# Kernel optimization log

Hardware: AMD Instinct MI355X
Metric: run time of the kernel (lower is better)

The kernel has to match this reference:

```python
import jax, jax.numpy as jnp
import numpy as np

N = 262144
DIM = 256
NUM_HEADS = 4
HEAD_DIM = DIM // NUM_HEADS
B = 4096
SCALE = HEAD_DIM ** (-0.5)
EPS = 1e-8


def setup_inputs() -> dict:
    key = jax.random.key(0)
    ks = jax.random.split(key, 7)
    x = jax.random.normal(ks[0], (N, DIM), dtype=jnp.float32)
    batch = jnp.sort(jax.random.randint(ks[1], (N,), 0, B)).astype(jnp.int64)
    query = jax.random.normal(ks[2], (NUM_HEADS, HEAD_DIM), dtype=jnp.float32)
    # nn.Linear default init scale ~ 1/sqrt(dim); keep exp() well-behaved
    key_w = jax.random.normal(ks[3], (DIM, DIM), dtype=jnp.float32) / np.sqrt(DIM)
    key_b = jax.random.normal(ks[4], (DIM,), dtype=jnp.float32) * 0.01
    value_w = jax.random.normal(ks[5], (DIM, DIM), dtype=jnp.float32) / np.sqrt(DIM)
    value_b = jax.random.normal(ks[6], (DIM,), dtype=jnp.float32) * 0.01
    return {"x": x, "batch": batch, "query": query, "key_w": key_w,
            "key_b": key_b, "value_w": value_w, "value_b": value_b}


def reference(x, batch, query, key_w, key_b, value_w, value_b):
    # k, v: [N, H, Hd]  (torch Linear: x @ W.T + b)
    k = (x @ key_w.T + key_b).reshape(N, NUM_HEADS, HEAD_DIM)
    v = (x @ value_w.T + value_b).reshape(N, NUM_HEADS, HEAD_DIM)
    # attn: [N, H] -- dot of learned per-head query with each node's key
    attn = jnp.einsum('hd,nhd->nh', query, k) * SCALE
    attn_exp = jnp.exp(attn)  # faithful: no max-subtraction in original
    # segment softmax denominator gathered back to nodes: [N, H]
    attn_sum = jax.ops.segment_sum(attn_exp, batch, num_segments=B)[batch]
    attn_norm = attn_exp / (attn_sum + EPS)
    # weighted values scatter-added per segment: [B, H, Hd]
    weighted = attn_norm[:, :, None] * v
    pooled = jax.ops.segment_sum(weighted, batch, num_segments=B)
    return pooled.reshape(B, DIM)
```

## Files before the change

### kernel.cpp

```cpp
#include <hip/hip_runtime.h>


constexpr int DIM = 256;
constexpr int NH  = 4;
constexpr int HD  = 64;
constexpr int G   = 8;
constexpr float SCL  = 0.125f;
constexpr float EPSV = 1e-8f;

constexpr int WS_QW   = 0;
constexpr int WS_QB   = 1024;
constexpr int WS_OFFS = 1088;
constexpr int WS_VWT  = 8192;

template<int CTRL>
__device__ __forceinline__ float dpp_ror_add(float v){
  int r = __builtin_amdgcn_update_dpp(0, __float_as_int(v), CTRL, 0xF, 0xF, false);
  return v + __int_as_float(r);
}
__device__ __forceinline__ float red32(float v){
  v = dpp_ror_add<0x121>(v);
  v = dpp_ror_add<0x122>(v);
  v = dpp_ror_add<0x124>(v);
  v = dpp_ror_add<0x128>(v);
  int r = __builtin_amdgcn_ds_swizzle(__float_as_int(v), 0x401F);
  return v + __int_as_float(r);
}

__global__ void prep_seg(const float* __restrict__ query,
                         const float* __restrict__ key_w,
                         const float* __restrict__ key_b,
                         const float* __restrict__ value_w,
                         const int* __restrict__ batch32,
                         float* __restrict__ ws,
                         int* __restrict__ offs,
                         int N, int B, int do_vwt){
  const int bid = blockIdx.x, tid = threadIdx.x;
  if (bid < 64){
    if (do_vwt){
      float4 v = *(const float4*)(value_w + (size_t)tid*DIM + 4*bid);
      ((float4*)(ws + WS_VWT))[bid*256 + tid] = v;
    }
  } else if (bid < 68){
    int t = (bid - 64)*256 + tid;
    int h = t >> 8, j = t & 255;
    float acc = 0.f;
    #pragma unroll 8
    for (int d = 0; d < HD; ++d)
      acc += query[h*HD+d] * key_w[(size_t)(h*HD+d)*DIM + j];
    ws[WS_QW + t] = acc;
    if (j == 0){
      float bb = 0.f;
      for (int d = 0; d < HD; ++d)
        bb += query[h*HD+d] * key_b[h*HD+d];
      ws[WS_QB + h] = bb;
    }
  } else {
    int i = (bid - 68)*256 + tid;
    if (i >= N) return;
    const bool is64 = (batch32[N-1] == 0);
    int v  = is64 ? batch32[2*i] : batch32[i];
    int vp = (i == 0) ? -1 : (is64 ? batch32[2*(i-1)] : batch32[i-1]);
    for (int b = vp + 1; b <= v; ++b) offs[b] = i;
    if (i == N-1)
      for (int b = v + 1; b <= B; ++b) offs[b] = N;
  }
}

__global__ __launch_bounds__(512, 4)
void attn_g8(const float* __restrict__ x,
             const int* __restrict__ offs,
             const float* __restrict__ ws,
             const float* __restrict__ value_b,
             float* __restrict__ out){
  __shared__ __align__(16) float S_all[8][1024];
  __shared__ __align__(16) float Sfin[G][1024];
  __shared__ float sums_all[8][NH];
  __shared__ float invs[G][NH], wsums[G][NH];

  const int b0  = blockIdx.x * G;
  const int tid = threadIdx.x;
  const int wave = tid >> 6, lane = tid & 63;
  const int half = lane >> 5, sl = lane & 31;
  const int sigma = wave * 2 + half;

  float qwr[NH][8];
  #pragma unroll
  for (int h = 0; h < NH; ++h){
    float4 a = *(const float4*)(ws + WS_QW + h*DIM + 4*sl);
    float4 c = *(const float4*)(ws + WS_QW + h*DIM + 128 + 4*sl);
    qwr[h][0]=a.x; qwr[h][1]=a.y; qwr[h][2]=a.z; qwr[h][3]=a.w;
    qwr[h][4]=c.x; qwr[h][5]=c.y; qwr[h][6]=c.z; qwr[h][7]=c.w;
  }
  float qb[NH];
  #pragma unroll
  for (int h = 0; h < NH; ++h) qb[h] = ws[WS_QB + h];

  const float4* xr4 = (const float4*)x;
  const float4 Z = make_float4(0.f, 0.f, 0.f, 0.f);

  for (int g = 0; g < G; ++g){
    const int s = offs[b0 + g], e = offs[b0 + g + 1];

    float Sacc[NH][8];
    #pragma unroll
    for (int h = 0; h < NH; ++h)
      #pragma unroll
      for (int c = 0; c < 8; ++c) Sacc[h][c] = 0.f;
    float se[NH] = {0.f, 0.f, 0.f, 0.f};

    int n0 = s + sigma*2;
    bool v0 = n0 < e;
    bool v1 = n0 + 1 < e;
    float4 la0=Z, lb0=Z, la1=Z, lb1=Z;
    if (v0){ la0 = xr4[(size_t)n0*64 + sl];     lb0 = xr4[(size_t)n0*64 + 32 + sl]; }
    if (v1){ la1 = xr4[(size_t)(n0+1)*64 + sl]; lb1 = xr4[(size_t)(n0+1)*64 + 32 + sl]; }

    while (v0){
      const int nn = n0 + 32;
      const bool w0 = nn < e;
      const bool w1 = nn + 1 < e;
      float4 nc0=Z, nd0=Z, nc1=Z, nd1=Z;
      if (w0){ nc0 = xr4[(size_t)nn*64 + sl];     nd0 = xr4[(size_t)nn*64 + 32 + sl]; }
      if (w1){ nc1 = xr4[(size_t)(nn+1)*64 + sl]; nd1 = xr4[(size_t)(nn+1)*64 + 32 + sl]; }

      float xv0[8] = {la0.x,la0.y,la0.z,la0.w,lb0.x,lb0.y,lb0.z,lb0.w};
      float xv1[8] = {la1.x,la1.y,la1.z,la1.w,lb1.x,lb1.y,lb1.z,lb1.w};

      float p0[NH], p1[NH];
      #pragma unroll
      for (int h = 0; h < NH; ++h){
        float s0 = 0.f, s1 = 0.f;
        #pragma unroll
        for (int c = 0; c < 8; ++c){ s0 += qwr[h][c]*xv0[c]; s1 += qwr[h][c]*xv1[c]; }
        p0[h] = s0; p1[h] = s1;
      }
      #pragma unroll
      for (int h = 0; h < NH; ++h){
        p0[h] = red32(p0[h]);
        p1[h] = red32(p1[h]);
      }
      const float g1 = v1 ? 1.f : 0.f;
      #pragma unroll
      for (int h = 0; h < NH; ++h){
        float e0 = __expf((p0[h] + qb[h]) * SCL);
        float e1 = __expf((p1[h] + qb[h]) * SCL) * g1;
        se[h] += e0 + e1;
        #pragma unroll
        for (int c = 0; c < 8; ++c)
          Sacc[h][c] += e0*xv0[c] + e1*xv1[c];
      }
      n0 = nn; v0 = w0; v1 = w1;
      la0 = nc0; lb0 = nd0; la1 = nc1; lb1 = nd1;
    }

    #pragma unroll
    for (int h = 0; h < NH; ++h){
      se[h] += __shfl_xor(se[h], 32, 64);
      #pragma unroll
      for (int c = 0; c < 8; ++c) Sacc[h][c] += __shfl_xor(Sacc[h][c], 32, 64);
    }
    if (half == 0){
      #pragma unroll
      for (int h = 0; h < NH; ++h){
        float4 lo = make_float4(Sacc[h][0], Sacc[h][1], Sacc[h][2], Sacc[h][3]);
        float4 hi = make_float4(Sacc[h][4], Sacc[h][5], Sacc[h][6], Sacc[h][7]);
        *(float4*)&S_all[wave][h*DIM + 4*sl]       = lo;
        *(float4*)&S_all[wave][h*DIM + 128 + 4*sl] = hi;
      }
      if (sl == 0){
        #pragma unroll
        for (int h = 0; h < NH; ++h) sums_all[wave][h] = se[h];
      }
    }
    __syncthreads();

    #pragma unroll
    for (int k2 = 0; k2 < 2; ++k2){
      const int idx = tid + k2*512;
      float sv = 0.f;
      #pragma unroll
      for (int w = 0; w < 8; ++w) sv += S_all[w][idx];
      Sfin[g][idx] = sv;
    }
    if (tid < NH){
      float tot = 0.f;
      #pragma unroll
      for (int w = 0; w < 8; ++w) tot += sums_all[w][tid];
      float inv = 1.f / (tot + EPSV);
      invs[g][tid]  = inv;
      wsums[g][tid] = tot * inv;
    }
    __syncthreads();
  }

  const int t = tid & 255, part = tid >> 8, h = t >> 6;
  const float4* vwt4 = (const float4*)(ws + WS_VWT);
  float acc[G];
  #pragma unroll
  for (int g = 0; g < G; ++g) acc[g] = 0.f;

  #pragma unroll 4
  for (int jj = part*32; jj < part*32 + 32; ++jj){
    const float4 w4 = vwt4[jj*256 + t];
    #pragma unroll
    for (int g = 0; g < G; ++g){
      const float4 s4 = *(const float4*)&Sfin[g][h*256 + 4*jj];
      acc[g] += w4.x*s4.x + w4.y*s4.y + w4.z*s4.z + w4.w*s4.w;
    }
  }
  float* ep = &S_all[0][0];
  #pragma unroll
  for (int g = 0; g < G; ++g) ep[(part*G + g)*256 + t] = acc[g];
  __syncthreads();
  if (part == 0){
    const float vb = value_b[t];
    #pragma unroll
    for (int g = 0; g < G; ++g){
      out[(size_t)(b0 + g)*256 + t] =
          (ep[g*256 + t] + ep[(G + g)*256 + t]) * invs[g][h] + wsums[g][h] * vb;
    }
  }
}

__global__ __launch_bounds__(512, 4)
void attn_pool_fused(const float* __restrict__ x,
                     const int* __restrict__ offs,
                     const float* __restrict__ ws,
                     const float* __restrict__ value_w,
                     const float* __restrict__ value_b,
                     float* __restrict__ out){
  __shared__ __align__(16) float lds[8192 + 32 + 1024 + 512 + 8];
  float* S_all    = lds;
  float* sums_all = lds + 8192;

  const int b   = blockIdx.x;
  const int tid = threadIdx.x;
  const int seg_start = offs[b];
  const int seg_end   = offs[b+1];

  const int wave = tid >> 6, lane = tid & 63;
  const int half = lane >> 5, sl = lane & 31;
  const int sigma = wave * 2 + half;

  float qwr[NH][8];
  #pragma unroll
  for (int h = 0; h < NH; ++h){
    float4 a = *(const float4*)(ws + WS_QW + h*DIM + 4*sl);
    float4 c = *(const float4*)(ws + WS_QW + h*DIM + 128 + 4*sl);
    qwr[h][0]=a.x; qwr[h][1]=a.y; qwr[h][2]=a.z; qwr[h][3]=a.w;
    qwr[h][4]=c.x; qwr[h][5]=c.y; qwr[h][6]=c.z; qwr[h][7]=c.w;
  }
  float qb[NH];
  #pragma unroll
  for (int h = 0; h < NH; ++h) qb[h] = ws[WS_QB + h];

  float Sacc[NH][8];
  #pragma unroll
  for (int h = 0; h < NH; ++h)
    #pragma unroll
    for (int c = 0; c < 8; ++c) Sacc[h][c] = 0.f;
  float se[NH] = {0.f, 0.f, 0.f, 0.f};

  const float4* xr4 = (const float4*)x;
  const float4 Z = make_float4(0.f,0.f,0.f,0.f);

  int n0 = seg_start + sigma*2;
  bool v0 = n0 < seg_end;
  bool v1 = n0 + 1 < seg_end;
  float4 a0=Z, b0=Z, a1=Z, b1=Z;
  if (v0){ a0 = xr4[(size_t)n0*64 + sl];     b0 = xr4[(size_t)n0*64 + 32 + sl]; }
  if (v1){ a1 = xr4[(size_t)(n0+1)*64 + sl]; b1 = xr4[(size_t)(n0+1)*64 + 32 + sl]; }

  while (v0){
    const int nn = n0 + 32;
    const bool w0 = nn < seg_end;
    const bool w1 = nn + 1 < seg_end;
    float4 c0=Z, d0=Z, c1=Z, d1=Z;
    if (w0){ c0 = xr4[(size_t)nn*64 + sl];     d0 = xr4[(size_t)nn*64 + 32 + sl]; }
    if (w1){ c1 = xr4[(size_t)(nn+1)*64 + sl]; d1 = xr4[(size_t)(nn+1)*64 + 32 + sl]; }

    float xv0[8] = {a0.x,a0.y,a0.z,a0.w,b0.x,b0.y,b0.z,b0.w};
    float xv1[8] = {a1.x,a1.y,a1.z,a1.w,b1.x,b1.y,b1.z,b1.w};

    float p0[NH], p1[NH];
    #pragma unroll
    for (int h = 0; h < NH; ++h){
      float s0 = 0.f, s1 = 0.f;
      #pragma unroll
      for (int c = 0; c < 8; ++c){ s0 += qwr[h][c]*xv0[c]; s1 += qwr[h][c]*xv1[c]; }
      p0[h] = s0; p1[h] = s1;
    }
    #pragma unroll
    for (int m = 1; m < 32; m <<= 1){
      #pragma unroll
      for (int h = 0; h < NH; ++h){
        p0[h] += __shfl_xor(p0[h], m, 64);
        p1[h] += __shfl_xor(p1[h], m, 64);
      }
    }
    const float g1 = v1 ? 1.f : 0.f;
    #pragma unroll
    for (int h = 0; h < NH; ++h){
      float e0 = __expf((p0[h] + qb[h]) * SCL);
      float e1 = __expf((p1[h] + qb[h]) * SCL) * g1;
      se[h] += e0 + e1;
      #pragma unroll
      for (int c = 0; c < 8; ++c)
        Sacc[h][c] += e0*xv0[c] + e1*xv1[c];
    }
    n0 = nn; v0 = w0; v1 = w1;
    a0 = c0; b0 = d0; a1 = c1; b1 = d1;
  }

  #pragma unroll
  for (int h = 0; h < NH; ++h){
    se[h] += __shfl_xor(se[h], 32, 64);
    #pragma unroll
    for (int c = 0; c < 8; ++c) Sacc[h][c] += __shfl_xor(Sacc[h][c], 32, 64);
  }
  if (half == 0){
    #pragma unroll
    for (int h = 0; h < NH; ++h){
      float4 lo = make_float4(Sacc[h][0], Sacc[h][1], Sacc[h][2], Sacc[h][3]);
      float4 hi = make_float4(Sacc[h][4], Sacc[h][5], Sacc[h][6], Sacc[h][7]);
      *(float4*)&S_all[wave*1024 + h*DIM + 4*sl]       = lo;
      *(float4*)&S_all[wave*1024 + h*DIM + 128 + 4*sl] = hi;
    }
    if (sl == 0){
      #pragma unroll
      for (int h = 0; h < NH; ++h) sums_all[wave*4 + h] = se[h];
    }
  }
  __syncthreads();

  float* Sfin  = lds + 8224;
  float* invs  = lds + 9760;
  float* wsums = invs + 4;
  #pragma unroll
  for (int k = 0; k < 2; ++k){
    const int idx = tid + k*512;
    float sv = 0.f;
    #pragma unroll
    for (int w = 0; w < 8; ++w) sv += S_all[w*1024 + idx];
    Sfin[idx] = sv;
  }
  if (tid < NH){
    float tot = 0.f;
    #pragma unroll
    for (int w = 0; w < 8; ++w) tot += sums_all[w*4 + tid];
    float inv = 1.f / (tot + EPSV);
    invs[tid] = inv; wsums[tid] = tot * inv;
  }
  __syncthreads();

  float* ep2 = lds + 9248;
  const int t = tid & 255, part = tid >> 8;
  const int h2 = t >> 6;
  const float4* vrow = (const float4*)(value_w + (size_t)t * DIM) + part*32;
  const float4* sp   = (const float4*)&Sfin[h2*256] + part*32;
  float acc = 0.f;
  #pragma unroll
  for (int q = 0; q < 32; ++q){
    float4 r = vrow[q];
    float4 sv = sp[q];
    acc += r.x*sv.x + r.y*sv.y + r.z*sv.z + r.w*sv.w;
  }
  ep2[part*256 + t] = acc;
  __syncthreads();
  if (part == 0)
    out[(size_t)b * DIM + t] = (ep2[t] + ep2[256 + t]) * invs[h2] + wsums[h2] * value_b[t];
}

extern "C" void kernel_launch(void* const* d_in, const int* in_sizes, int n_in,
                              void* d_out, int out_size, void* d_ws, size_t ws_size,
                              hipStream_t stream){
  const float* x       = (const float*)d_in[0];
  const int*   batch   = (const int*)d_in[1];
  const float* query   = (const float*)d_in[2];
  const float* key_w   = (const float*)d_in[3];
  const float* key_b   = (const float*)d_in[4];
  const float* value_w = (const float*)d_in[5];
  const float* value_b = (const float*)d_in[6];
  float* ws  = (float*)d_ws;
  float* out = (float*)d_out;

  const int N = in_sizes[1];
  const int B = out_size / DIM;

  int* offs = (int*)(ws + WS_OFFS);

  const size_t need_vwt = ((size_t)WS_VWT + 65536) * sizeof(float);
  const int do_vwt = (ws_size >= need_vwt) ? 1 : 0;

  const int seg_blocks = (N + 255) / 256;
  prep_seg<<<68 + seg_blocks, 256, 0, stream>>>(query, key_w, key_b, value_w,
                                                batch, ws, offs, N, B, do_vwt);
  if (do_vwt && (B % G) == 0)
    attn_g8<<<B / G, 512, 0, stream>>>(x, offs, ws, value_b, out);
  else
    attn_pool_fused<<<B, 512, 0, stream>>>(x, offs, ws, value_w, value_b, out);
}
```

Measured before the change: 402.2 us.

## Fuse prep into single attention kernel with per-block binary search and qW recompute

Replaces the prep kernel plus grouped attention kernel with a single kernel that finds segment offsets by binary search over the batch array, recomputes query·key_w into LDS per block, and reads value_w rows directly instead of a transposed workspace copy. This removes one kernel launch and the global offset and transpose passes. In exchange every block redundantly computes the 1024-element qW product (64 MACs per element, reading key_w), and value_w is now read row-wise per thread, which is uncoalesced. The fallback path also switches to the DPP reduction.

```diff
diff --git a/kernel.cpp b/kernel.cpp
--- a/kernel.cpp
+++ b/kernel.cpp
@@ -4,14 +4,12 @@
 constexpr int DIM = 256;
 constexpr int NH  = 4;
 constexpr int HD  = 64;
-constexpr int G   = 8;
 constexpr float SCL  = 0.125f;
 constexpr float EPSV = 1e-8f;
 
 constexpr int WS_QW   = 0;
 constexpr int WS_QB   = 1024;
 constexpr int WS_OFFS = 1088;
-constexpr int WS_VWT  = 8192;
 
 template<int CTRL>
 __device__ __forceinline__ float dpp_ror_add(float v){
@@ -27,22 +25,209 @@
   return v + __int_as_float(r);
 }
 
+__global__ __launch_bounds__(512, 4)
+void attn_all(const float* __restrict__ x,
+              const int* __restrict__ batch32,
+              const float* __restrict__ query,
+              const float* __restrict__ key_w,
+              const float* __restrict__ key_b,
+              const float* __restrict__ value_w,
+              const float* __restrict__ value_b,
+              float* __restrict__ out,
+              int N, int B){
+  constexpr int G8 = 8;
+  __shared__ __align__(16) float S_all[8][1024];
+  __shared__ __align__(16) float Sfin[G8][1024];
+  __shared__ __align__(16) float qwL[1024];
+  __shared__ float qbL[NH];
+  __shared__ float sums_all[8][NH];
+  __shared__ float invs[G8][NH], wsums[G8][NH];
+  __shared__ int offsL[G8 + 1];
+
+  const int bid = blockIdx.x, tid = threadIdx.x;
+  const int b0  = bid * G8;
+
+  const bool is64 = (batch32[N-1] == 0);
+  if (tid <= G8){
+    const int target = b0 + tid;
+    int lo = 0, hi = N;
+    while (lo < hi){
+      const int mid = (lo + hi) >> 1;
+      const int v = is64 ? batch32[2*(size_t)mid] : batch32[mid];
+      if (v < target) lo = mid + 1; else hi = mid;
+    }
+    offsL[tid] = lo;
+  }
+
+  for (int idx = tid; idx < 1024; idx += 512){
+    const int h = idx >> 8, j = idx & 255;
+    float acc = 0.f;
+    #pragma unroll 8
+    for (int d = 0; d < HD; ++d)
+      acc += query[h*HD+d] * key_w[(size_t)(h*HD+d)*DIM + j];
+    qwL[idx] = acc;
+  }
+  if (tid < NH){
+    float bb = 0.f;
+    for (int d = 0; d < HD; ++d)
+      bb += query[tid*HD+d] * key_b[tid*HD+d];
+    qbL[tid] = bb;
+  }
+  __syncthreads();
+
+  const int wave = tid >> 6, lane = tid & 63;
+  const int half = lane >> 5, sl = lane & 31;
+  const int sigma = wave * 2 + half;
+
+  float qwr[NH][8];
+  #pragma unroll
+  for (int h = 0; h < NH; ++h){
+    float4 a = *(const float4*)&qwL[h*DIM + 4*sl];
+    float4 c = *(const float4*)&qwL[h*DIM + 128 + 4*sl];
+    qwr[h][0]=a.x; qwr[h][1]=a.y; qwr[h][2]=a.z; qwr[h][3]=a.w;
+    qwr[h][4]=c.x; qwr[h][5]=c.y; qwr[h][6]=c.z; qwr[h][7]=c.w;
+  }
+  float qb[NH];
+  #pragma unroll
+  for (int h = 0; h < NH; ++h) qb[h] = qbL[h];
+
+  const float4* xr4 = (const float4*)x;
+  const float4 Z = make_float4(0.f, 0.f, 0.f, 0.f);
+
+  for (int g = 0; g < G8; ++g){
+    const int s = offsL[g], e = offsL[g+1];
+
+    float Sacc[NH][8];
+    #pragma unroll
+    for (int h = 0; h < NH; ++h)
+      #pragma unroll
+      for (int c = 0; c < 8; ++c) Sacc[h][c] = 0.f;
+    float se[NH] = {0.f, 0.f, 0.f, 0.f};
+
+    int n0 = s + sigma*2;
+    bool v0 = n0 < e;
+    bool v1 = n0 + 1 < e;
+    float4 la0=Z, lb0=Z, la1=Z, lb1=Z;
+    if (v0){ la0 = xr4[(size_t)n0*64 + sl];     lb0 = xr4[(size_t)n0*64 + 32 + sl]; }
+    if (v1){ la1 = xr4[(size_t)(n0+1)*64 + sl]; lb1 = xr4[(size_t)(n0+1)*64 + 32 + sl]; }
+
+    while (v0){
+      const int nn = n0 + 32;
+      const bool w0 = nn < e;
+      const bool w1 = nn + 1 < e;
+      float4 nc0=Z, nd0=Z, nc1=Z, nd1=Z;
+      if (w0){ nc0 = xr4[(size_t)nn*64 + sl];     nd0 = xr4[(size_t)nn*64 + 32 + sl]; }
+      if (w1){ nc1 = xr4[(size_t)(nn+1)*64 + sl]; nd1 = xr4[(size_t)(nn+1)*64 + 32 + sl]; }
+
+      float xv0[8] = {la0.x,la0.y,la0.z,la0.w,lb0.x,lb0.y,lb0.z,lb0.w};
+      float xv1[8] = {la1.x,la1.y,la1.z,la1.w,lb1.x,lb1.y,lb1.z,lb1.w};
+
+      float p0[NH], p1[NH];
+      #pragma unroll
+      for (int h = 0; h < NH; ++h){
+        float s0 = 0.f, s1 = 0.f;
+        #pragma unroll
+        for (int c = 0; c < 8; ++c){ s0 += qwr[h][c]*xv0[c]; s1 += qwr[h][c]*xv1[c]; }
+        p0[h] = s0; p1[h] = s1;
+      }
+      #pragma unroll
+      for (int h = 0; h < NH; ++h){
+        p0[h] = red32(p0[h]);
+        p1[h] = red32(p1[h]);
+      }
+      const float g1 = v1 ? 1.f : 0.f;
+      #pragma unroll
+      for (int h = 0; h < NH; ++h){
+        float e0 = __expf((p0[h] + qb[h]) * SCL);
+        float e1 = __expf((p1[h] + qb[h]) * SCL) * g1;
+        se[h] += e0 + e1;
+        #pragma unroll
+        for (int c = 0; c < 8; ++c)
+          Sacc[h][c] += e0*xv0[c] + e1*xv1[c];
+      }
+      n0 = nn; v0 = w0; v1 = w1;
+      la0 = nc0; lb0 = nd0; la1 = nc1; lb1 = nd1;
+    }
+
+    #pragma unroll
+    for (int h = 0; h < NH; ++h){
+      se[h] += __shfl_xor(se[h], 32, 64);
+      #pragma unroll
+      for (int c = 0; c < 8; ++c) Sacc[h][c] += __shfl_xor(Sacc[h][c], 32, 64);
+    }
+    if (half == 0){
+      #pragma unroll
+      for (int h = 0; h < NH; ++h){
+        float4 lo = make_float4(Sacc[h][0], Sacc[h][1], Sacc[h][2], Sacc[h][3]);
+        float4 hi = make_float4(Sacc[h][4], Sacc[h][5], Sacc[h][6], Sacc[h][7]);
+        *(float4*)&S_all[wave][h*DIM + 4*sl]       = lo;
+        *(float4*)&S_all[wave][h*DIM + 128 + 4*sl] = hi;
+      }
+      if (sl == 0){
+        #pragma unroll
+        for (int h = 0; h < NH; ++h) sums_all[wave][h] = se[h];
+      }
+    }
+    __syncthreads();
+
+    #pragma unroll
+    for (int k2 = 0; k2 < 2; ++k2){
+      const int idx = tid + k2*512;
+      float sv = 0.f;
+      #pragma unroll
+      for (int w = 0; w < 8; ++w) sv += S_all[w][idx];
+      Sfin[g][idx] = sv;
+    }
+    if (tid < NH){
+      float tot = 0.f;
+      #pragma unroll
+      for (int w = 0; w < 8; ++w) tot += sums_all[w][tid];
+      float inv = 1.f / (tot + EPSV);
+      invs[g][tid]  = inv;
+      wsums[g][tid] = tot * inv;
+    }
+    __syncthreads();
+  }
+
+  const int t = tid & 255, part = tid >> 8, h = t >> 6;
+  const float4* vrow = (const float4*)(value_w + (size_t)t * DIM) + part*32;
+  float acc[G8];
+  #pragma unroll
+  for (int g = 0; g < G8; ++g) acc[g] = 0.f;
+
+  for (int q = 0; q < 32; ++q){
+    const float4 r = vrow[q];
+    const int jj = part*32 + q;
+    #pragma unroll
+    for (int g = 0; g < G8; ++g){
+      const float4 s4 = *(const float4*)&Sfin[g][h*256 + 4*jj];
+      acc[g] += r.x*s4.x + r.y*s4.y + r.z*s4.z + r.w*s4.w;
+    }
+  }
+  float* ep = &S_all[0][0];
+  #pragma unroll
+  for (int g = 0; g < G8; ++g) ep[(part*G8 + g)*256 + t] = acc[g];
+  __syncthreads();
+  if (part == 0){
+    const float vb = value_b[t];
+    #pragma unroll
+    for (int g = 0; g < G8; ++g){
+      out[(size_t)(b0 + g)*256 + t] =
+          (ep[g*256 + t] + ep[(G8 + g)*256 + t]) * invs[g][h] + wsums[g][h] * vb;
+    }
+  }
+}
+
 __global__ void prep_seg(const float* __restrict__ query,
                          const float* __restrict__ key_w,
                          const float* __restrict__ key_b,
-                         const float* __restrict__ value_w,
                          const int* __restrict__ batch32,
                          float* __restrict__ ws,
                          int* __restrict__ offs,
-                         int N, int B, int do_vwt){
+                         int N, int B){
   const int bid = blockIdx.x, tid = threadIdx.x;
-  if (bid < 64){
-    if (do_vwt){
-      float4 v = *(const float4*)(value_w + (size_t)tid*DIM + 4*bid);
-      ((float4*)(ws + WS_VWT))[bid*256 + tid] = v;
-    }
-  } else if (bid < 68){
-    int t = (bid - 64)*256 + tid;
+  if (bid < 4){
+    int t = bid*256 + tid;
     int h = t >> 8, j = t & 255;
     float acc = 0.f;
     #pragma unroll 8
@@ -56,7 +241,7 @@
       ws[WS_QB + h] = bb;
     }
   } else {
-    int i = (bid - 68)*256 + tid;
+    int i = (bid - 4)*256 + tid;
     if (i >= N) return;
     const bool is64 = (batch32[N-1] == 0);
     int v  = is64 ? batch32[2*i] : batch32[i];
@@ -64,162 +249,6 @@
     for (int b = vp + 1; b <= v; ++b) offs[b] = i;
     if (i == N-1)
       for (int b = v + 1; b <= B; ++b) offs[b] = N;
-  }
-}
-
-__global__ __launch_bounds__(512, 4)
-void attn_g8(const float* __restrict__ x,
-             const int* __restrict__ offs,
-             const float* __restrict__ ws,
-             const float* __restrict__ value_b,
-             float* __restrict__ out){
-  __shared__ __align__(16) float S_all[8][1024];
-  __shared__ __align__(16) float Sfin[G][1024];
-  __shared__ float sums_all[8][NH];
-  __shared__ float invs[G][NH], wsums[G][NH];
-
-  const int b0  = blockIdx.x * G;
-  const int tid = threadIdx.x;
-  const int wave = tid >> 6, lane = tid & 63;
-  const int half = lane >> 5, sl = lane & 31;
-  const int sigma = wave * 2 + half;
-
-  float qwr[NH][8];
-  #pragma unroll
-  for (int h = 0; h < NH; ++h){
-    float4 a = *(const float4*)(ws + WS_QW + h*DIM + 4*sl);
-    float4 c = *(const float4*)(ws + WS_QW + h*DIM + 128 + 4*sl);
-    qwr[h][0]=a.x; qwr[h][1]=a.y; qwr[h][2]=a.z; qwr[h][3]=a.w;
-    qwr[h][4]=c.x; qwr[h][5]=c.y; qwr[h][6]=c.z; qwr[h][7]=c.w;
-  }
-  float qb[NH];
-  #pragma unroll
-  for (int h = 0; h < NH; ++h) qb[h] = ws[WS_QB + h];
-
-  const float4* xr4 = (const float4*)x;
-  const float4 Z = make_float4(0.f, 0.f, 0.f, 0.f);
-
-  for (int g = 0; g < G; ++g){
-    const int s = offs[b0 + g], e = offs[b0 + g + 1];
-
-    float Sacc[NH][8];
-    #pragma unroll
-    for (int h = 0; h < NH; ++h)
-      #pragma unroll
-      for (int c = 0; c < 8; ++c) Sacc[h][c] = 0.f;
-    float se[NH] = {0.f, 0.f, 0.f, 0.f};
-
-    int n0 = s + sigma*2;
-    bool v0 = n0 < e;
-    bool v1 = n0 + 1 < e;
-    float4 la0=Z, lb0=Z, la1=Z, lb1=Z;
-    if (v0){ la0 = xr4[(size_t)n0*64 + sl];     lb0 = xr4[(size_t)n0*64 + 32 + sl]; }
-    if (v1){ la1 = xr4[(size_t)(n0+1)*64 + sl]; lb1 = xr4[(size_t)(n0+1)*64 + 32 + sl]; }
-
-    while (v0){
-      const int nn = n0 + 32;
-      const bool w0 = nn < e;
-      const bool w1 = nn + 1 < e;
-      float4 nc0=Z, nd0=Z, nc1=Z, nd1=Z;
-      if (w0){ nc0 = xr4[(size_t)nn*64 + sl];     nd0 = xr4[(size_t)nn*64 + 32 + sl]; }
-      if (w1){ nc1 = xr4[(size_t)(nn+1)*64 + sl]; nd1 = xr4[(size_t)(nn+1)*64 + 32 + sl]; }
-
-      float xv0[8] = {la0.x,la0.y,la0.z,la0.w,lb0.x,lb0.y,lb0.z,lb0.w};
-      float xv1[8] = {la1.x,la1.y,la1.z,la1.w,lb1.x,lb1.y,lb1.z,lb1.w};
-
-      float p0[NH], p1[NH];
-      #pragma unroll
-      for (int h = 0; h < NH; ++h){
-        float s0 = 0.f, s1 = 0.f;
-        #pragma unroll
-        for (int c = 0; c < 8; ++c){ s0 += qwr[h][c]*xv0[c]; s1 += qwr[h][c]*xv1[c]; }
-        p0[h] = s0; p1[h] = s1;
-      }
-      #pragma unroll
-      for (int h = 0; h < NH; ++h){
-        p0[h] = red32(p0[h]);
-        p1[h] = red32(p1[h]);
-      }
-      const float g1 = v1 ? 1.f : 0.f;
-      #pragma unroll
-      for (int h = 0; h < NH; ++h){
-        float e0 = __expf((p0[h] + qb[h]) * SCL);
-        float e1 = __expf((p1[h] + qb[h]) * SCL) * g1;
-        se[h] += e0 + e1;
-        #pragma unroll
-        for (int c = 0; c < 8; ++c)
-          Sacc[h][c] += e0*xv0[c] + e1*xv1[c];
-      }
-      n0 = nn; v0 = w0; v1 = w1;
-      la0 = nc0; lb0 = nd0; la1 = nc1; lb1 = nd1;
-    }
-
-    #pragma unroll
-    for (int h = 0; h < NH; ++h){
-      se[h] += __shfl_xor(se[h], 32, 64);
-      #pragma unroll
-      for (int c = 0; c < 8; ++c) Sacc[h][c] += __shfl_xor(Sacc[h][c], 32, 64);
-    }
-    if (half == 0){
-      #pragma unroll
-      for (int h = 0; h < NH; ++h){
-        float4 lo = make_float4(Sacc[h][0], Sacc[h][1], Sacc[h][2], Sacc[h][3]);
-        float4 hi = make_float4(Sacc[h][4], Sacc[h][5], Sacc[h][6], Sacc[h][7]);
-        *(float4*)&S_all[wave][h*DIM + 4*sl]       = lo;
-        *(float4*)&S_all[wave][h*DIM + 128 + 4*sl] = hi;
-      }
-      if (sl == 0){
-        #pragma unroll
-        for (int h = 0; h < NH; ++h) sums_all[wave][h] = se[h];
-      }
-    }
-    __syncthreads();
-
-    #pragma unroll
-    for (int k2 = 0; k2 < 2; ++k2){
-      const int idx = tid + k2*512;
-      float sv = 0.f;
-      #pragma unroll
-      for (int w = 0; w < 8; ++w) sv += S_all[w][idx];
-      Sfin[g][idx] = sv;
-    }
-    if (tid < NH){
-      float tot = 0.f;
-      #pragma unroll
-      for (int w = 0; w < 8; ++w) tot += sums_all[w][tid];
-      float inv = 1.f / (tot + EPSV);
-      invs[g][tid]  = inv;
-      wsums[g][tid] = tot * inv;
-    }
-    __syncthreads();
-  }
-
-  const int t = tid & 255, part = tid >> 8, h = t >> 6;
-  const float4* vwt4 = (const float4*)(ws + WS_VWT);
-  float acc[G];
-  #pragma unroll
-  for (int g = 0; g < G; ++g) acc[g] = 0.f;
-
-  #pragma unroll 4
-  for (int jj = part*32; jj < part*32 + 32; ++jj){
-    const float4 w4 = vwt4[jj*256 + t];
-    #pragma unroll
-    for (int g = 0; g < G; ++g){
-      const float4 s4 = *(const float4*)&Sfin[g][h*256 + 4*jj];
-      acc[g] += w4.x*s4.x + w4.y*s4.y + w4.z*s4.z + w4.w*s4.w;
-    }
-  }
-  float* ep = &S_all[0][0];
-  #pragma unroll
-  for (int g = 0; g < G; ++g) ep[(part*G + g)*256 + t] = acc[g];
-  __syncthreads();
-  if (part == 0){
-    const float vb = value_b[t];
-    #pragma unroll
-    for (int g = 0; g < G; ++g){
-      out[(size_t)(b0 + g)*256 + t] =
-          (ep[g*256 + t] + ep[(G + g)*256 + t]) * invs[g][h] + wsums[g][h] * vb;
-    }
   }
 }
 
@@ -292,12 +321,9 @@
       p0[h] = s0; p1[h] = s1;
     }
     #pragma unroll
-    for (int m = 1; m < 32; m <<= 1){
-      #pragma unroll
-      for (int h = 0; h < NH; ++h){
-        p0[h] += __shfl_xor(p0[h], m, 64);
-        p1[h] += __shfl_xor(p1[h], m, 64);
-      }
+    for (int h = 0; h < NH; ++h){
+      p0[h] = red32(p0[h]);
+      p1[h] = red32(p1[h]);
     }
     const float g1 = v1 ? 1.f : 0.f;
     #pragma unroll
@@ -385,19 +411,17 @@
   float* ws  = (float*)d_ws;
   float* out = (float*)d_out;
 
-  const int N = in_sizes[1];
-  const int B = out_size / DIM;
-
-  int* offs = (int*)(ws + WS_OFFS);
-
-  const size_t need_vwt = ((size_t)WS_VWT + 65536) * sizeof(float);
-  const int do_vwt = (ws_size >= need_vwt) ? 1 : 0;
-
-  const int seg_blocks = (N + 255) / 256;
-  prep_seg<<<68 + seg_blocks, 256, 0, stream>>>(query, key_w, key_b, value_w,
-                                                batch, ws, offs, N, B, do_vwt);
-  if (do_vwt && (B % G) == 0)
-    attn_g8<<<B / G, 512, 0, stream>>>(x, offs, ws, value_b, out);
-  else
+  int N = in_sizes[1];
+  int B = out_size / DIM;
+
+  if ((B % 8) == 0){
+    attn_all<<<B / 8, 512, 0, stream>>>(x, batch, query, key_w, key_b,
+                                        value_w, value_b, out, N, B);
+  } else {
+    int* offs = (int*)(ws + WS_OFFS);
+    const int seg_blocks = (N + 255) / 256;
+    prep_seg<<<4 + seg_blocks, 256, 0, stream>>>(query, key_w, key_b,
+                                                 batch, ws, offs, N, B);
     attn_pool_fused<<<B, 512, 0, stream>>>(x, offs, ws, value_w, value_b, out);
-}
+  }
+}
```

Result: slower. 413.6 us (+2.8%).
